# Performance work log

Measured on AMD Instinct MI355X. Metric: run time of the kernel, lower is better.

The kernel has to match this reference:

```python
import jax, jax.numpy as jnp
import numpy as np

EPS = 1e-8


def _cos_distance(a, b):
    # a, b: [1, c, hw] ; centered cosine distance matrix [1, hw, hw2]
    a = a - a.mean(axis=2, keepdims=True)
    b = b - b.mean(axis=2, keepdims=True)
    a_norm = jnp.sqrt((a * a).sum(axis=1, keepdims=True) + EPS)
    b_norm = jnp.sqrt((b * b).sum(axis=1, keepdims=True) + EPS)
    a = a / (a_norm + EPS)
    b = b / (b_norm + EPS)
    return 1.0 - jnp.einsum('bci,bcj->bij', a, b)


def _cos_loss(a, b):
    # a, b: [1, c, hw]; mean of (1 - cosine similarity along channel dim)
    a_norm = jnp.sqrt((a * a).sum(axis=1, keepdims=True))
    b_norm = jnp.sqrt((b * b).sum(axis=1, keepdims=True))
    a_t = a / (a_norm + EPS)
    b_t = b / (b_norm + EPS)
    cossim = (a_t * b_t).sum(axis=1)
    return (1.0 - cossim).mean()


def setup_inputs() -> dict:
    key = jax.random.key(0)
    k1, k2 = jax.random.split(key)
    x_feats = jax.random.normal(k1, (1, 768, 128, 128), dtype=jnp.float32)
    s_feats = jax.random.normal(k2, (1, 768, 128, 128), dtype=jnp.float32)
    return {"x_feats": x_feats, "s_feats": s_feats}


def reference(x_feats, s_feats):
    n, c, h, w = x_feats.shape
    a_flat = x_feats.reshape(n, c, h * w)          # [1, c, hw]
    b_flat = s_feats.reshape(n, c, -1)             # [1, c, hw2]
    # cdist + argmin retrieval (feat_replace)
    d_mat = _cos_distance(a_flat, b_flat)          # [1, hw, hw2] (~1 GB)
    z_best = jnp.argmin(d_mat, axis=2)             # [1, hw]
    target = b_flat[:, :, z_best[0]]               # gather NN swap -> [1, c, hw]
    # cosine loss between x feats and NN-replaced target feats
    nn_loss = _cos_loss(a_flat, target)
    return nn_loss
```

## Files before the change

kernel.cpp:

```cpp
#include <hip/hip_runtime.h>
#include <hip/hip_bf16.h>
#include <stdint.h>

#define C_DIM 768
#define HW 16384
#define EPSF 1e-8f
#define GPQ 256

typedef __attribute__((ext_vector_type(4))) int i32x4;

__global__ __launch_bounds__(256) void k_means(const float* __restrict__ x,
                                               const float* __restrict__ s,
                                               float* __restrict__ meanA,
                                               float* __restrict__ meanB) {
  int ch = blockIdx.x;
  const float* src = (ch < C_DIM) ? (x + (size_t)ch * HW) : (s + (size_t)(ch - C_DIM) * HW);
  const float4* src4 = (const float4*)src;
  int t = threadIdx.x;
  float acc = 0.f;
  for (int i = t; i < HW / 4; i += 256) {
    float4 v = src4[i];
    acc += v.x + v.y + v.z + v.w;
  }
  __shared__ float red[256];
  red[t] = acc;
  __syncthreads();
  for (int o = 128; o > 0; o >>= 1) {
    if (t < o) red[t] += red[t + o];
    __syncthreads();
  }
  if (t == 0) {
    float m = red[0] * (1.0f / HW);
    if (ch < C_DIM) meanA[ch] = m; else meanB[ch - C_DIM] = m;
  }
}

__global__ __launch_bounds__(256) void k_prepq(const float* __restrict__ x,
                                               const float* __restrict__ s,
                                               const float* __restrict__ meanA,
                                               const float* __restrict__ meanB,
                                               float* __restrict__ qsaG,
                                               float* __restrict__ effG,
                                               float* __restrict__ invbnG,
                                               float* __restrict__ rawNA,
                                               float* __restrict__ rawNB,
                                               float* __restrict__ uG,
                                               float* __restrict__ vG,
                                               signed char* __restrict__ qa,
                                               signed char* __restrict__ Bp) {
  __shared__ float lma[C_DIM], lmb[C_DIM];
  __shared__ float red[7 * 256];
  __shared__ signed char tA8[64 * 40];
  __shared__ signed char tB8[64 * 40];
  __shared__ float lsa[64], lsb[64];
  int t = threadIdx.x;
  int j0 = blockIdx.x * 64;
  for (int c = t; c < C_DIM; c += 256) { lma[c] = meanA[c]; lmb[c] = meanB[c]; }
  __syncthreads();

  {
    int pl = t & 63, cl = t >> 6;
    int p = j0 + pl;
    float maxa = 0.f, ssaR = 0.f, maxb = 0.f, ssbC = 0.f, ssbR = 0.f, uacc = 0.f, vacc = 0.f;
    for (int c = cl; c < C_DIM; c += 4) {
      float av = x[(size_t)c * HW + p];
      float bv = s[(size_t)c * HW + p];
      float ac = av - lma[c];
      float bc = bv - lmb[c];
      maxa = fmaxf(maxa, fabsf(ac));
      maxb = fmaxf(maxb, fabsf(bc));
      ssaR += av * av;
      ssbC += bc * bc;
      ssbR += bv * bv;
      uacc += ac * lmb[c];
      vacc += bc * lma[c];
    }
    red[t] = maxa; red[256 + t] = ssaR; red[512 + t] = maxb;
    red[768 + t] = ssbC; red[1024 + t] = ssbR; red[1280 + t] = uacc; red[1536 + t] = vacc;
    __syncthreads();
    if (t < 64) {
      float ma = fmaxf(fmaxf(red[t], red[t + 64]), fmaxf(red[t + 128], red[t + 192]));
      float sa = red[256 + t] + red[256 + t + 64] + red[256 + t + 128] + red[256 + t + 192];
      float mb = fmaxf(fmaxf(red[512 + t], red[512 + t + 64]), fmaxf(red[512 + t + 128], red[512 + t + 192]));
      float sc = red[768 + t] + red[768 + t + 64] + red[768 + t + 128] + red[768 + t + 192];
      float sb = red[1024 + t] + red[1024 + t + 64] + red[1024 + t + 128] + red[1024 + t + 192];
      float uu = red[1280 + t] + red[1280 + t + 64] + red[1280 + t + 128] + red[1280 + t + 192];
      float vv = red[1536 + t] + red[1536 + t + 64] + red[1536 + t + 128] + red[1536 + t + 192];
      ma = fmaxf(ma, 1e-20f);
      mb = fmaxf(mb, 1e-20f);
      float ib = 1.0f / (sqrtf(sc + EPSF) + EPSF);
      lsa[t] = 127.0f / ma;
      lsb[t] = 127.0f / mb;
      qsaG[j0 + t] = 127.0f / ma;
      effG[j0 + t] = (mb * (1.0f / 127.0f)) * ib;
      invbnG[j0 + t] = ib;
      rawNA[j0 + t] = sqrtf(sa);
      rawNB[j0 + t] = sqrtf(sb);
      uG[j0 + t] = uu;
      vG[j0 + t] = vv;
    }
  }
  __syncthreads();

  int cc = t & 63;
  int r4 = t >> 6;
  float sa = lsa[cc];
  float sb = lsb[cc];
  int pS = t >> 2;
  int ch8 = (t & 3) * 8;
  int pgS = j0 + pS;
  int gS = pgS >> 4, laneS = pgS & 15;

  for (int c0 = 0; c0 < C_DIM; c0 += 32) {
    __syncthreads();
#pragma unroll
    for (int v = 0; v < 2; ++v) {
      int q4 = r4 + 4 * v;
      unsigned pa = 0, pb = 0;
#pragma unroll
      for (int uu = 0; uu < 4; ++uu) {
        int c = c0 + q4 * 4 + uu;
        float av = (x[(size_t)c * HW + j0 + cc] - lma[c]) * sa;
        float bv = (s[(size_t)c * HW + j0 + cc] - lmb[c]) * sb;
        int qA = (int)rintf(fminf(fmaxf(av, -127.f), 127.f));
        int qB = (int)rintf(fminf(fmaxf(bv, -127.f), 127.f));
        pa |= ((unsigned)(unsigned char)(signed char)qA) << (8 * uu);
        pb |= ((unsigned)(unsigned char)(signed char)qB) << (8 * uu);
      }
      *(unsigned*)&tA8[cc * 40 + q4 * 4] = pa;
      *(unsigned*)&tB8[cc * 40 + q4 * 4] = pb;
    }
    __syncthreads();
    unsigned long long va = *(const unsigned long long*)&tA8[pS * 40 + ch8];
    *(unsigned long long*)(qa + (size_t)pgS * C_DIM + c0 + ch8) = va;
    unsigned long long vb = *(const unsigned long long*)&tB8[pS * 40 + ch8];
    int k0 = c0 + ch8;
    int sblk = k0 >> 6;
    int quad = (k0 & 63) >> 4;
    int e0 = k0 & 15;
    *(unsigned long long*)(Bp + (size_t)(gS * 12 + sblk) * 1024 + (laneS | (quad << 4)) * 16 + e0) = vb;
  }
}

__device__ __forceinline__ void gl_lds16(const void* g, void* l) {
  __builtin_amdgcn_global_load_lds((const __attribute__((address_space(1))) uint32_t*)g,
                                   (__attribute__((address_space(3))) uint32_t*)l, 16, 0, 0);
}

__global__ __launch_bounds__(256, 2) void k_gemm_argmax(
    const signed char* __restrict__ qa,
    const signed char* __restrict__ Bp,
    const float* __restrict__ eff,
    unsigned long long* __restrict__ best) {
  __shared__ signed char ringS[4 * 12288];
  __shared__ float effL[4096];
  int t = threadIdx.x;
  int lane = t & 63, w = t >> 6;
  int m = lane & 15, q = lane >> 4;
  int b = blockIdx.x;
  int xcd = b & 7;
  int bq = xcd >> 1;
  int rg = (b >> 3) | ((xcd & 1) << 6);
  int i0 = rg * 128;
  int g0 = bq * GPQ;
  int lane16 = lane * 16;
  int sW0 = (3 * w) * 1024 + lane16;

  const i32x4* qaV = (const i32x4*)qa;
  i32x4 a_res[2][12];
#pragma unroll
  for (int tm = 0; tm < 2; ++tm) {
    int row = i0 + w * 32 + tm * 16 + m;
#pragma unroll
    for (int s = 0; s < 12; ++s)
      a_res[tm][s] = qaV[(size_t)row * 48 + s * 4 + q];
  }

  {
    const signed char* ps = Bp + ((size_t)g0 * 12 + 3 * w) * 1024 + lane16;
#pragma unroll
    for (int gp = 0; gp < 3; ++gp) {
      signed char* dst = ringS + gp * 12288;
      gl_lds16(ps, dst + sW0);
      gl_lds16(ps + 1024, dst + sW0 + 1024);
      gl_lds16(ps + 2048, dst + sW0 + 2048);
      ps += 12288;
    }
  }
  for (int i = t; i < 4096; i += 256) effL[i] = eff[(g0 << 4) + i];
  __syncthreads();

  const signed char* srcW = Bp + ((size_t)(g0 + 3) * 12 + 3 * w) * 1024 + lane16;

  float bestv[2][4];
  int bestj[2][4];
#pragma unroll
  for (int tm = 0; tm < 2; ++tm)
#pragma unroll
    for (int r = 0; r < 4; ++r) { bestv[tm][r] = -3.0e38f; bestj[tm][r] = 0x7FFFFFFF; }

  int effOff = m;
  int jj = (g0 << 4) + m;

  i32x4 fA[6], fB[6];
#pragma unroll
  for (int s = 0; s < 6; ++s) fA[s] = *(const i32x4*)(ringS + s * 1024 + lane16);

#define BODY(SLOT, VMSTR, DOSTAGE, DOAHEAD)                                        \
  {                                                                                \
    asm volatile(VMSTR ::: "memory");                                              \
    __builtin_amdgcn_s_barrier();                                                  \
    const signed char* rb = ringS + (SLOT) * 12288;                                \
    _Pragma("unroll")                                                              \
    for (int s = 0; s < 6; ++s)                                                    \
      fB[s] = *(const i32x4*)(rb + (6 + s) * 1024 + lane16);                       \
    if (DOSTAGE) {                                                                 \
      signed char* dst = ringS + (((SLOT) + 3) & 3) * 12288;                       \
      gl_lds16(srcW, dst + sW0);                                                   \
      gl_lds16(srcW + 1024, dst + sW0 + 1024);                                     \
      gl_lds16(srcW + 2048, dst + sW0 + 2048);                                     \
      srcW += 12288;                                                               \
    }                                                                              \
    i32x4 acc0 = {0, 0, 0, 0}, acc1 = {0, 0, 0, 0};                                \
    _Pragma("unroll")                                                              \
    for (int s = 0; s < 6; ++s) {                                                  \
      acc0 = __builtin_amdgcn_mfma_i32_16x16x64_i8(a_res[0][s], fA[s], acc0, 0, 0, 0); \
      acc1 = __builtin_amdgcn_mfma_i32_16x16x64_i8(a_res[1][s], fA[s], acc1, 0, 0, 0); \
    }                                                                              \
    if (DOAHEAD) {                                                                 \
      const signed char* rn = ringS + (((SLOT) + 1) & 3) * 12288;                  \
      _Pragma("unroll")                                                            \
      for (int s = 0; s < 6; ++s)                                                  \
        fA[s] = *(const i32x4*)(rn + s * 1024 + lane16);                           \
    }                                                                              \
    _Pragma("unroll")                                                              \
    for (int s = 0; s < 6; ++s) {                                                  \
      acc0 = __builtin_amdgcn_mfma_i32_16x16x64_i8(a_res[0][6 + s], fB[s], acc0, 0, 0, 0); \
      acc1 = __builtin_amdgcn_mfma_i32_16x16x64_i8(a_res[1][6 + s], fB[s], acc1, 0, 0, 0); \
    }                                                                              \
    float ecur = effL[effOff];                                                     \
    _Pragma("unroll")                                                              \
    for (int r = 0; r < 4; ++r) {                                                  \
      float v0 = (float)acc0[r] * ecur;                                            \
      float v1 = (float)acc1[r] * ecur;                                            \
      if (v0 > bestv[0][r]) { bestv[0][r] = v0; bestj[0][r] = jj; }                \
      if (v1 > bestv[1][r]) { bestv[1][r] = v1; bestj[1][r] = jj; }                \
    }                                                                              \
    effOff += 16;                                                                  \
    jj += 16;                                                                      \
  }

  for (int mi = 0; mi < 63; ++mi) {
    BODY(0, "s_waitcnt vmcnt(3)", 1, 1)
    BODY(1, "s_waitcnt vmcnt(3)", 1, 1)
    BODY(2, "s_waitcnt vmcnt(3)", 1, 1)
    BODY(3, "s_waitcnt vmcnt(3)", 1, 1)
  }
  BODY(0, "s_waitcnt vmcnt(3)", 1, 1)
  BODY(1, "s_waitcnt vmcnt(3)", 0, 1)
  BODY(2, "s_waitcnt vmcnt(0)", 0, 1)
  BODY(3, "s_waitcnt vmcnt(0)", 0, 0)
#undef BODY

#pragma unroll
  for (int tm = 0; tm < 2; ++tm) {
#pragma unroll
    for (int r = 0; r < 4; ++r) {
      float bv = bestv[tm][r];
      int bj = bestj[tm][r];
#pragma unroll
      for (int off = 1; off < 16; off <<= 1) {
        float ov = __shfl_xor(bv, off, 64);
        int oj = __shfl_xor(bj, off, 64);
        if (ov > bv || (ov == bv && oj < bj)) { bv = ov; bj = oj; }
      }
      if (m == 0) {
        int i = i0 + w * 32 + tm * 16 + q * 4 + r;
        unsigned key = __float_as_uint(bv);
        key = (key & 0x80000000u) ? ~key : (key | 0x80000000u);
        unsigned long long packed =
            ((unsigned long long)key << 32) | (unsigned long long)(0xFFFFFFFFu - (unsigned)bj);
        atomicMax(&best[i], packed);
      }
    }
  }
}

__global__ __launch_bounds__(256) void k_loss2(const float* __restrict__ meanA,
                                               const float* __restrict__ meanB,
                                               const unsigned long long* __restrict__ best,
                                               const float* __restrict__ rawNA,
                                               const float* __restrict__ rawNB,
                                               const float* __restrict__ invbn,
                                               const float* __restrict__ qsa,
                                               const float* __restrict__ u,
                                               const float* __restrict__ v,
                                               float* __restrict__ out) {
  __shared__ float red[256];
  int t = threadIdx.x;
  float wp = 0.f;
  for (int c = t; c < C_DIM; c += 256) wp += meanA[c] * meanB[c];
  red[t] = wp;
  __syncthreads();
  for (int o = 128; o > 0; o >>= 1) {
    if (t < o) red[t] += red[t + o];
    __syncthreads();
  }
  float wdot = red[0];
  __syncthreads();

  int i = blockIdx.x * 256 + t;
  unsigned long long pk = best[i];
  unsigned key = (unsigned)(pk >> 32);
  unsigned fb = (key & 0x80000000u) ? (key & 0x7FFFFFFFu) : ~key;
  float bv = __uint_as_float(fb);
  int j = (int)(0xFFFFFFFFu - (unsigned)(pk & 0xFFFFFFFFull));
  float dotcc = bv / (invbn[j] * qsa[i]);
  float dot = dotcc + u[i] + v[j] + wdot;
  float cs = dot / ((rawNA[i] + EPSF) * (rawNB[j] + EPSF));
  red[t] = (1.0f - cs) * (1.0f / HW);
  __syncthreads();
  for (int o = 128; o > 0; o >>= 1) {
    if (t < o) red[t] += red[t + o];
    __syncthreads();
  }
  if (t == 0) atomicAdd(out, red[0]);
}

extern "C" void kernel_launch(void* const* d_in, const int* in_sizes, int n_in,
                              void* d_out, int out_size, void* d_ws, size_t ws_size,
                              hipStream_t stream) {
  const float* x = (const float*)d_in[0];
  const float* s = (const float*)d_in[1];
  char* ws = (char*)d_ws;
  float* meanA = (float*)(ws + 0);
  float* meanB = (float*)(ws + 4096);
  float* rawNA = (float*)(ws + 8192);
  float* rawNB = (float*)(ws + 73728);
  float* eff   = (float*)(ws + 139264);
  float* qsa   = (float*)(ws + 204800);
  float* invbn = (float*)(ws + 335872);
  float* u     = (float*)(ws + 401408);
  float* v     = (float*)(ws + 466944);
  unsigned long long* best = (unsigned long long*)(ws + 532480);
  signed char* qa = (signed char*)(ws + 663552);
  signed char* Bp = (signed char*)(ws + 663552 + 12582912);
  float* out = (float*)d_out;

  hipMemsetAsync(best, 0, HW * sizeof(unsigned long long), stream);
  hipMemsetAsync(out, 0, sizeof(float), stream);
  k_means<<<2 * C_DIM, 256, 0, stream>>>(x, s, meanA, meanB);
  k_prepq<<<HW / 64, 256, 0, stream>>>(x, s, meanA, meanB, qsa, eff, invbn, rawNA, rawNB, u, v, qa, Bp);
  k_gemm_argmax<<<512, 256, 0, stream>>>(qa, Bp, eff, best);
  k_loss2<<<HW / 256, 256, 0, stream>>>(meanA, meanB, best, rawNA, rawNB, invbn, qsa, u, v, out);
}
```

Before: 393.3 us.

## Enlarge row tile per wave and pack argmax value and index into 32 bits

Each wave now holds 64 A rows (4 MFMA row tiles) instead of 32, so every B fragment loaded from LDS feeds four MFMAs, and each block covers 128 column groups with a 3-slot LDS ring. The per-lane argmax keeps one 32-bit key: the order-preserving float bits with the low 14 bits replaced by a column tag. This drops the separate index registers and the compare/select pairs, and lets the final reduction use a 32-bit atomicMax. The cost is more register pressure from 48 resident A fragments, and dropping the low 14 mantissa bits coarsens the comparison, which can pick a different argmax among near-ties.

```diff
diff --git a/kernel.cpp b/kernel.cpp
--- a/kernel.cpp
+++ b/kernel.cpp
@@ -5,7 +5,7 @@
 #define C_DIM 768
 #define HW 16384
 #define EPSF 1e-8f
-#define GPQ 256
+#define GPP 128
 
 typedef __attribute__((ext_vector_type(4))) int i32x4;
 
@@ -151,26 +151,25 @@
     const signed char* __restrict__ qa,
     const signed char* __restrict__ Bp,
     const float* __restrict__ eff,
-    unsigned long long* __restrict__ best) {
-  __shared__ signed char ringS[4 * 12288];
-  __shared__ float effL[4096];
+    unsigned* __restrict__ best) {
+  __shared__ signed char ringS[3 * 12288];
+  __shared__ float effL[2048];
   int t = threadIdx.x;
   int lane = t & 63, w = t >> 6;
   int m = lane & 15, q = lane >> 4;
   int b = blockIdx.x;
-  int xcd = b & 7;
-  int bq = xcd >> 1;
-  int rg = (b >> 3) | ((xcd & 1) << 6);
-  int i0 = rg * 128;
-  int g0 = bq * GPQ;
+  int part = b & 7;
+  int rg = b >> 3;
+  int i0 = rg * 256;
+  int g0 = part * GPP;
   int lane16 = lane * 16;
   int sW0 = (3 * w) * 1024 + lane16;
 
   const i32x4* qaV = (const i32x4*)qa;
-  i32x4 a_res[2][12];
-#pragma unroll
-  for (int tm = 0; tm < 2; ++tm) {
-    int row = i0 + w * 32 + tm * 16 + m;
+  i32x4 a_res[4][12];
+#pragma unroll
+  for (int tm = 0; tm < 4; ++tm) {
+    int row = i0 + w * 64 + tm * 16 + m;
 #pragma unroll
     for (int s = 0; s < 12; ++s)
       a_res[tm][s] = qaV[(size_t)row * 48 + s * 4 + q];
@@ -179,7 +178,7 @@
   {
     const signed char* ps = Bp + ((size_t)g0 * 12 + 3 * w) * 1024 + lane16;
 #pragma unroll
-    for (int gp = 0; gp < 3; ++gp) {
+    for (int gp = 0; gp < 2; ++gp) {
       signed char* dst = ringS + gp * 12288;
       gl_lds16(ps, dst + sW0);
       gl_lds16(ps + 1024, dst + sW0 + 1024);
@@ -187,100 +186,91 @@
       ps += 12288;
     }
   }
-  for (int i = t; i < 4096; i += 256) effL[i] = eff[(g0 << 4) + i];
-  __syncthreads();
-
-  const signed char* srcW = Bp + ((size_t)(g0 + 3) * 12 + 3 * w) * 1024 + lane16;
-
-  float bestv[2][4];
-  int bestj[2][4];
-#pragma unroll
-  for (int tm = 0; tm < 2; ++tm)
-#pragma unroll
-    for (int r = 0; r < 4; ++r) { bestv[tm][r] = -3.0e38f; bestj[tm][r] = 0x7FFFFFFF; }
-
-  int effOff = m;
-  int jj = (g0 << 4) + m;
-
-  i32x4 fA[6], fB[6];
-#pragma unroll
-  for (int s = 0; s < 6; ++s) fA[s] = *(const i32x4*)(ringS + s * 1024 + lane16);
-
-#define BODY(SLOT, VMSTR, DOSTAGE, DOAHEAD)                                        \
+  for (int i = t; i < 2048; i += 256) effL[i] = eff[(g0 << 4) + i];
+  __syncthreads();
+
+  const signed char* srcW = Bp + ((size_t)(g0 + 2) * 12 + 3 * w) * 1024 + lane16;
+
+  unsigned best16[4][4];
+#pragma unroll
+  for (int tm = 0; tm < 4; ++tm)
+#pragma unroll
+    for (int r = 0; r < 4; ++r) best16[tm][r] = 0u;
+
+  unsigned tag = ((unsigned)(1023 - g0) << 4) | (unsigned)(15 - m);
+  int effIdx = m;
+
+#define BODY(SLOT, VMSTR, DOSTAGE)                                                 \
   {                                                                                \
     asm volatile(VMSTR ::: "memory");                                              \
     __builtin_amdgcn_s_barrier();                                                  \
     const signed char* rb = ringS + (SLOT) * 12288;                                \
-    _Pragma("unroll")                                                              \
-    for (int s = 0; s < 6; ++s)                                                    \
-      fB[s] = *(const i32x4*)(rb + (6 + s) * 1024 + lane16);                       \
     if (DOSTAGE) {                                                                 \
-      signed char* dst = ringS + (((SLOT) + 3) & 3) * 12288;                       \
+      signed char* dst = ringS + (((SLOT) + 2) % 3) * 12288;                       \
       gl_lds16(srcW, dst + sW0);                                                   \
       gl_lds16(srcW + 1024, dst + sW0 + 1024);                                     \
       gl_lds16(srcW + 2048, dst + sW0 + 2048);                                     \
       srcW += 12288;                                                               \
     }                                                                              \
-    i32x4 acc0 = {0, 0, 0, 0}, acc1 = {0, 0, 0, 0};                                \
+    i32x4 acc0 = {0,0,0,0}, acc1 = {0,0,0,0}, acc2 = {0,0,0,0}, acc3 = {0,0,0,0};  \
+    i32x4 fa = *(const i32x4*)(rb + lane16);                                       \
+    i32x4 fb = *(const i32x4*)(rb + 1024 + lane16);                                \
     _Pragma("unroll")                                                              \
-    for (int s = 0; s < 6; ++s) {                                                  \
-      acc0 = __builtin_amdgcn_mfma_i32_16x16x64_i8(a_res[0][s], fA[s], acc0, 0, 0, 0); \
-      acc1 = __builtin_amdgcn_mfma_i32_16x16x64_i8(a_res[1][s], fA[s], acc1, 0, 0, 0); \
+    for (int s = 0; s < 12; ++s) {                                                 \
+      i32x4 fn = fb;                                                               \
+      if (s < 10) fn = *(const i32x4*)(rb + (s + 2) * 1024 + lane16);              \
+      acc0 = __builtin_amdgcn_mfma_i32_16x16x64_i8(a_res[0][s], fa, acc0, 0, 0, 0); \
+      acc1 = __builtin_amdgcn_mfma_i32_16x16x64_i8(a_res[1][s], fa, acc1, 0, 0, 0); \
+      acc2 = __builtin_amdgcn_mfma_i32_16x16x64_i8(a_res[2][s], fa, acc2, 0, 0, 0); \
+      acc3 = __builtin_amdgcn_mfma_i32_16x16x64_i8(a_res[3][s], fa, acc3, 0, 0, 0); \
+      fa = fb; fb = fn;                                                            \
     }                                                                              \
-    if (DOAHEAD) {                                                                 \
-      const signed char* rn = ringS + (((SLOT) + 1) & 3) * 12288;                  \
-      _Pragma("unroll")                                                            \
-      for (int s = 0; s < 6; ++s)                                                  \
-        fA[s] = *(const i32x4*)(rn + s * 1024 + lane16);                           \
-    }                                                                              \
-    _Pragma("unroll")                                                              \
-    for (int s = 0; s < 6; ++s) {                                                  \
-      acc0 = __builtin_amdgcn_mfma_i32_16x16x64_i8(a_res[0][6 + s], fB[s], acc0, 0, 0, 0); \
-      acc1 = __builtin_amdgcn_mfma_i32_16x16x64_i8(a_res[1][6 + s], fB[s], acc1, 0, 0, 0); \
-    }                                                                              \
-    float ecur = effL[effOff];                                                     \
+    float ecur = effL[effIdx];                                                     \
     _Pragma("unroll")                                                              \
     for (int r = 0; r < 4; ++r) {                                                  \
       float v0 = (float)acc0[r] * ecur;                                            \
       float v1 = (float)acc1[r] * ecur;                                            \
-      if (v0 > bestv[0][r]) { bestv[0][r] = v0; bestj[0][r] = jj; }                \
-      if (v1 > bestv[1][r]) { bestv[1][r] = v1; bestj[1][r] = jj; }                \
+      float v2 = (float)acc2[r] * ecur;                                            \
+      float v3 = (float)acc3[r] * ecur;                                            \
+      unsigned u0 = __float_as_uint(v0); u0 = (u0 & 0x80000000u) ? ~u0 : (u0 | 0x80000000u); \
+      unsigned u1 = __float_as_uint(v1); u1 = (u1 & 0x80000000u) ? ~u1 : (u1 | 0x80000000u); \
+      unsigned u2 = __float_as_uint(v2); u2 = (u2 & 0x80000000u) ? ~u2 : (u2 | 0x80000000u); \
+      unsigned u3 = __float_as_uint(v3); u3 = (u3 & 0x80000000u) ? ~u3 : (u3 | 0x80000000u); \
+      u0 = (u0 & 0xFFFFC000u) | tag;                                               \
+      u1 = (u1 & 0xFFFFC000u) | tag;                                               \
+      u2 = (u2 & 0xFFFFC000u) | tag;                                               \
+      u3 = (u3 & 0xFFFFC000u) | tag;                                               \
+      if (u0 > best16[0][r]) best16[0][r] = u0;                                    \
+      if (u1 > best16[1][r]) best16[1][r] = u1;                                    \
+      if (u2 > best16[2][r]) best16[2][r] = u2;                                    \
+      if (u3 > best16[3][r]) best16[3][r] = u3;                                    \
     }                                                                              \
-    effOff += 16;                                                                  \
-    jj += 16;                                                                      \
-  }
-
-  for (int mi = 0; mi < 63; ++mi) {
-    BODY(0, "s_waitcnt vmcnt(3)", 1, 1)
-    BODY(1, "s_waitcnt vmcnt(3)", 1, 1)
-    BODY(2, "s_waitcnt vmcnt(3)", 1, 1)
-    BODY(3, "s_waitcnt vmcnt(3)", 1, 1)
-  }
-  BODY(0, "s_waitcnt vmcnt(3)", 1, 1)
-  BODY(1, "s_waitcnt vmcnt(3)", 0, 1)
-  BODY(2, "s_waitcnt vmcnt(0)", 0, 1)
-  BODY(3, "s_waitcnt vmcnt(0)", 0, 0)
+    tag -= 16u;                                                                    \
+    effIdx += 16;                                                                  \
+  }
+
+  for (int it = 0; it < 42; ++it) {
+    BODY(0, "s_waitcnt vmcnt(3)", 1)
+    BODY(1, "s_waitcnt vmcnt(3)", 1)
+    BODY(2, "s_waitcnt vmcnt(3)", 1)
+  }
+  BODY(0, "s_waitcnt vmcnt(3)", 0)
+  BODY(1, "s_waitcnt vmcnt(0)", 0)
 #undef BODY
 
 #pragma unroll
-  for (int tm = 0; tm < 2; ++tm) {
+  for (int tm = 0; tm < 4; ++tm) {
 #pragma unroll
     for (int r = 0; r < 4; ++r) {
-      float bv = bestv[tm][r];
-      int bj = bestj[tm][r];
+      unsigned bv = best16[tm][r];
 #pragma unroll
       for (int off = 1; off < 16; off <<= 1) {
-        float ov = __shfl_xor(bv, off, 64);
-        int oj = __shfl_xor(bj, off, 64);
-        if (ov > bv || (ov == bv && oj < bj)) { bv = ov; bj = oj; }
+        unsigned ov = __shfl_xor(bv, off, 64);
+        if (ov > bv) bv = ov;
       }
       if (m == 0) {
-        int i = i0 + w * 32 + tm * 16 + q * 4 + r;
-        unsigned key = __float_as_uint(bv);
-        key = (key & 0x80000000u) ? ~key : (key | 0x80000000u);
-        unsigned long long packed =
-            ((unsigned long long)key << 32) | (unsigned long long)(0xFFFFFFFFu - (unsigned)bj);
-        atomicMax(&best[i], packed);
+        int i = i0 + w * 64 + tm * 16 + q * 4 + r;
+        atomicMax(&best[i], bv);
       }
     }
   }
@@ -288,7 +278,7 @@
 
 __global__ __launch_bounds__(256) void k_loss2(const float* __restrict__ meanA,
                                                const float* __restrict__ meanB,
-                                               const unsigned long long* __restrict__ best,
+                                               const unsigned* __restrict__ best,
                                                const float* __restrict__ rawNA,
                                                const float* __restrict__ rawNB,
                                                const float* __restrict__ invbn,
@@ -310,11 +300,14 @@
   __syncthreads();
 
   int i = blockIdx.x * 256 + t;
-  unsigned long long pk = best[i];
-  unsigned key = (unsigned)(pk >> 32);
-  unsigned fb = (key & 0x80000000u) ? (key & 0x7FFFFFFFu) : ~key;
-  float bv = __uint_as_float(fb);
-  int j = (int)(0xFFFFFFFFu - (unsigned)(pk & 0xFFFFFFFFull));
+  unsigned pk = best[i];
+  int tagv = (int)(pk & 0x3FFFu);
+  int g = 1023 - (tagv >> 4);
+  int mm = 15 - (tagv & 0xF);
+  int j = g * 16 + mm;
+  unsigned ou = pk & 0xFFFFC000u;
+  unsigned fu = (ou & 0x80000000u) ? (ou & 0x7FFFFFFFu) : ~ou;
+  float bv = __uint_as_float(fu);
   float dotcc = bv / (invbn[j] * qsa[i]);
   float dot = dotcc + u[i] + v[j] + wdot;
   float cs = dot / ((rawNA[i] + EPSF) * (rawNB[j] + EPSF));
@@ -342,12 +335,12 @@
   float* invbn = (float*)(ws + 335872);
   float* u     = (float*)(ws + 401408);
   float* v     = (float*)(ws + 466944);
-  unsigned long long* best = (unsigned long long*)(ws + 532480);
+  unsigned* best = (unsigned*)(ws + 532480);
   signed char* qa = (signed char*)(ws + 663552);
   signed char* Bp = (signed char*)(ws + 663552 + 12582912);
   float* out = (float*)d_out;
 
-  hipMemsetAsync(best, 0, HW * sizeof(unsigned long long), stream);
+  hipMemsetAsync(best, 0, HW * sizeof(unsigned), stream);
   hipMemsetAsync(out, 0, sizeof(float), stream);
   k_means<<<2 * C_DIM, 256, 0, stream>>>(x, s, meanA, meanB);
   k_prepq<<<HW / 64, 256, 0, stream>>>(x, s, meanA, meanB, qsa, eff, invbn, rawNA, rawNB, u, v, qa, Bp);
```

After: 508.7 us. 29.3% more time.
